# Performance work log

Measured on AMD Instinct MI355X. Metric: run time of the kernel, lower is better.

## Reference

```python
import jax, jax.numpy as jnp
import numpy as np

N_NODES = 50000


def gcn_layer(x, src, dst, ew, W, b, n_nodes):
    # PyG GCNConv: add self-loops (weight 1), symmetric deg^-1/2 normalization,
    # linear transform, scatter-add aggregation at destination, then bias.
    loop = jnp.arange(n_nodes, dtype=src.dtype)
    s = jnp.concatenate([src, loop])
    d = jnp.concatenate([dst, loop])
    w = jnp.concatenate([ew, jnp.ones((n_nodes,), dtype=ew.dtype)])
    deg = jax.ops.segment_sum(w, d, num_segments=n_nodes)  # [N]
    dinv = jnp.where(deg > 0, jax.lax.rsqrt(jnp.where(deg > 0, deg, 1.0)), 0.0)
    norm = dinv[s] * w * dinv[d]  # [E+N]
    h = x @ W  # [N, out]
    msg = h[s] * norm[:, None]  # gather + scale, [E+N, out]
    out = jax.ops.segment_sum(msg, d, num_segments=n_nodes)  # scatter-add
    return out + b


def setup_inputs() -> dict:
    key = jax.random.key(0)
    k1, k2, k3, k4, k5, k6, k7 = jax.random.split(key, 7)
    N, E, C_IN, C_OUT = N_NODES, 600000, 128, 128
    x = jax.random.normal(k1, (N, C_IN), dtype=jnp.float32)
    edge_index = jax.random.randint(k2, (2, E), 0, N, dtype=jnp.int64)
    edge_weight = jax.random.uniform(k3, (E,), dtype=jnp.float32)
    # Glorot-style init like PyG's Linear default
    s1 = 1.0 / np.sqrt(C_IN)
    s2 = 1.0 / np.sqrt(C_OUT)
    W1 = jax.random.uniform(k4, (C_IN, C_OUT), jnp.float32, -s1, s1)
    b1 = jnp.zeros((C_OUT,), dtype=jnp.float32)
    W2 = jax.random.uniform(k5, (C_OUT, C_OUT), jnp.float32, -s2, s2)
    b2 = jnp.zeros((C_OUT,), dtype=jnp.float32)
    return {"x": x, "edge_index": edge_index, "edge_weight": edge_weight,
            "W1": W1, "b1": b1, "W2": W2, "b2": b2}


def reference(x, edge_index, edge_weight, W1, b1, W2, b2):
    src, dst = edge_index[0], edge_index[1]
    h = jax.nn.relu(gcn_layer(x, src, dst, edge_weight, W1, b1, N_NODES))
    return jax.nn.relu(gcn_layer(h, src, dst, edge_weight, W2, b2, N_NODES))
```

## Files before the change

### kernel.cpp

```cpp
#include <hip/hip_runtime.h>
#include <math.h>

#define CH   128
#define CH4  32
#define TPB  256
#define SCANB 1024
#define WIMG 16384
#define NREP 8
#define FIXS 1048576.0f

typedef __attribute__((ext_vector_type(8))) short short8;
typedef __attribute__((ext_vector_type(4))) float floatx4;
typedef __attribute__((ext_vector_type(8))) float float8;
typedef unsigned long long u64;

static __device__ __forceinline__ unsigned short f2bf(float f) {
    unsigned u = __float_as_uint(f);
    return (unsigned short)((u + 0x7fffu + ((u >> 16) & 1u)) >> 16);
}
static __device__ __forceinline__ float bf2f(unsigned short s) {
    return __uint_as_float(((unsigned)s) << 16);
}
static __device__ __forceinline__ float8 bf8_to_f8(short8 u) {
    float8 f;
    #pragma unroll
    for (int i = 0; i < 8; ++i) f[i] = bf2f((unsigned short)u[i]);
    return f;
}
static __device__ __forceinline__ int xcc_id() {
    int x;
    asm volatile("s_getreg_b32 %0, hwreg(HW_REG_XCC_ID)" : "=s"(x));
    return x & (NREP - 1);
}

__global__ void k_prep(const float* __restrict__ W1, const float* __restrict__ W2,
                       short* __restrict__ Wsplit, float4* __restrict__ zbase,
                       int nzero4, int nbPrep) {
    int bx = blockIdx.x;
    if (bx >= nbPrep) {
        int i = (bx - nbPrep) * TPB + threadIdx.x;
        if (i < nzero4) zbase[i] = make_float4(0.f, 0.f, 0.f, 0.f);
        return;
    }
    int i = bx * TPB + threadIdx.x;
    if (i >= 2 * CH * CH) return;
    int layer = i >> 14;
    int idx   = i & 16383;
    int k = idx >> 7, c = idx & 127;
    float w = (layer ? W2 : W1)[k * CH + c];
    unsigned short hi = f2bf(w);
    unsigned short lo = f2bf(w - bf2f(hi));
    int colh = c >> 6, nn = c & 63;
    int kt = k >> 5, q = (k & 31) >> 3, j = k & 7;
    int ns = nn >> 4, ln = q * 16 + (nn & 15);
    size_t base = (size_t)(layer * 2 + colh) * WIMG;
    size_t off  = ((size_t)(kt * 4 + ns) * 64 + ln) * 8 + j;
    Wsplit[base + off]        = (short)hi;
    Wsplit[base + 8192 + off] = (short)lo;
}

static __device__ __forceinline__ void gemm_body_f32(
        const float* __restrict__ X, const short* __restrict__ Wfrag,
        unsigned short* __restrict__ H, int n, int tile, int colh, int tid) {
    __shared__ __align__(16) short sW[2][4][4][64][8];
    {
        const float4* gsrc = (const float4*)Wfrag;
        float4* ldst = (float4*)sW;
        #pragma unroll
        for (int i = 0; i < 8; ++i)
            ldst[i * TPB + tid] = gsrc[i * TPB + tid];
    }
    __syncthreads();

    const int lane = tid & 63;
    const int wv   = tid >> 6;
    const int q    = lane >> 4;
    const int m    = lane & 15;
    const int row0 = tile * 64 + wv * 16;
    if (row0 >= n) return;

    int rrow = row0 + m;
    if (rrow > n - 1) rrow = n - 1;

    const float4* xr = (const float4*)(X + (size_t)rrow * CH);
    float4 xa[4][2];
    #pragma unroll
    for (int kt = 0; kt < 4; ++kt) {
        xa[kt][0] = xr[kt * 8 + q * 2 + 0];
        xa[kt][1] = xr[kt * 8 + q * 2 + 1];
    }

    floatx4 acc[4];
    #pragma unroll
    for (int ns = 0; ns < 4; ++ns) acc[ns] = (floatx4){0.f, 0.f, 0.f, 0.f};

    #pragma unroll
    for (int kt = 0; kt < 4; ++kt) {
        float xf[8] = { xa[kt][0].x, xa[kt][0].y, xa[kt][0].z, xa[kt][0].w,
                        xa[kt][1].x, xa[kt][1].y, xa[kt][1].z, xa[kt][1].w };
        short8 ah, al;
        #pragma unroll
        for (int j = 0; j < 8; ++j) {
            float v = xf[j];
            unsigned short h = f2bf(v);
            ah[j] = (short)h;
            al[j] = (short)f2bf(v - bf2f(h));
        }
        #pragma unroll
        for (int ns = 0; ns < 4; ++ns) {
            short8 bh = *(const short8*)&sW[0][kt][ns][lane][0];
            short8 bl = *(const short8*)&sW[1][kt][ns][lane][0];
            acc[ns] = __builtin_amdgcn_mfma_f32_16x16x32_bf16(ah, bh, acc[ns], 0, 0, 0);
            acc[ns] = __builtin_amdgcn_mfma_f32_16x16x32_bf16(al, bh, acc[ns], 0, 0, 0);
            acc[ns] = __builtin_amdgcn_mfma_f32_16x16x32_bf16(ah, bl, acc[ns], 0, 0, 0);
        }
    }

    #pragma unroll
    for (int ns = 0; ns < 4; ++ns) {
        #pragma unroll
        for (int reg = 0; reg < 4; ++reg) {
            int r = row0 + q * 4 + reg;
            if (r < n)
                H[(size_t)r * CH + colh * 64 + ns * 16 + m] = f2bf(acc[ns][reg]);
        }
    }
}

__global__ __launch_bounds__(TPB, 4)
void k_gemm_rank(const float* __restrict__ X, const short* __restrict__ Wsplit,
                 unsigned short* __restrict__ H, int n,
                 const int* __restrict__ dst, const float* __restrict__ ew,
                 u64* __restrict__ counts_rep, int* __restrict__ rank,
                 int E, int nbE4, int Np) {
    int bx = blockIdx.x;
    if (bx < nbE4) {
        const int rep = xcc_id();
        int stride = nbE4 * TPB;
        int e = bx * TPB + threadIdx.x;
        #pragma unroll
        for (int it = 0; it < 4; ++it, e += stride) {
            if (e < E) {
                int d = dst[e];
                if ((unsigned)d < (unsigned)n) {
                    u64 pk = (1ull << 40) |
                             (u64)(unsigned)__float2uint_rn(ew[e] * FIXS);
                    u64 old = atomicAdd(&counts_rep[(size_t)rep * Np + d], pk);
                    rank[e] = (rep << 28) | (int)(old >> 40);
                }
            }
        }
    } else {
        bx -= nbE4;
        int colh = bx & 1;
        gemm_body_f32(X, Wsplit + (size_t)colh * WIMG, H, n, bx >> 1, colh,
                      threadIdx.x);
    }
}

__global__ __launch_bounds__(SCANB)
void k_scan1(const u64* __restrict__ counts_rep, int Np,
             int* __restrict__ counts_tot, int* __restrict__ repoff8,
             int* __restrict__ row_start, float* __restrict__ dinv,
             int* __restrict__ partials, int* __restrict__ pp_s,
             int* __restrict__ done, int nb, int n) {
    __shared__ int swt[SCANB / 64];
    __shared__ int slastS;
    const int tid  = threadIdx.x;
    const int lane = tid & 63;
    const int wid  = tid >> 6;
    const int gid  = blockIdx.x * SCANB + tid;

    int c[NREP];
    int v = 0;
    u64 wsum = 0;
    #pragma unroll
    for (int r = 0; r < NREP; ++r) {
        u64 pk = (gid < n) ? counts_rep[(size_t)r * Np + gid] : 0ull;
        c[r] = (int)(pk >> 40);
        wsum += pk & ((1ull << 40) - 1);
        v += c[r];
    }
    const int vp = (v + 7) & ~7;
    int inc = vp;
    #pragma unroll
    for (int off = 1; off < 64; off <<= 1) {
        int t = __shfl_up(inc, off, 64);
        if (lane >= off) inc += t;
    }
    if (lane == 63) swt[wid] = inc;
    __syncthreads();
    if (wid == 0) {
        int wv_ = (lane < SCANB / 64) ? swt[lane] : 0;
        int winc = wv_;
        #pragma unroll
        for (int off = 1; off < SCANB / 64; off <<= 1) {
            int t = __shfl_up(winc, off, 64);
            if (lane >= off) winc += t;
        }
        if (lane < SCANB / 64) swt[lane] = winc - wv_;
    }
    __syncthreads();
    const int myincl = inc + swt[wid];

    if (gid < n) {
        row_start[gid]  = myincl - vp;
        counts_tot[gid] = v;
        dinv[gid] = rsqrtf(1.0f + (float)wsum * (1.0f / FIXS));
        int pre = 0;
        int ro[NREP];
        #pragma unroll
        for (int r = 0; r < NREP; ++r) { ro[r] = pre; pre += c[r]; }
        ((int4*)repoff8)[gid * 2 + 0] = make_int4(ro[0], ro[1], ro[2], ro[3]);
        ((int4*)repoff8)[gid * 2 + 1] = make_int4(ro[4], ro[5], ro[6], ro[7]);
    }
    if (tid == SCANB - 1) {
        partials[blockIdx.x] = myincl;
        __threadfence();
        int old = atomicAdd(done, 1);
        slastS = (old == nb - 1);
    }
    __syncthreads();
    if (slastS && tid < 64) {
        int pv = (tid < nb) ? atomicAdd(&partials[tid], 0) : 0;
        int i2 = pv;
        #pragma unroll
        for (int off = 1; off < 64; off <<= 1) {
            int t = __shfl_up(i2, off, 64);
            if ((tid & 63) >= off) i2 += t;
        }
        if (tid < nb) pp_s[tid] = i2 - pv;
    }
}

__global__ void k_fill(const int* __restrict__ src, const int* __restrict__ dst,
                       const float* __restrict__ ew, const int* __restrict__ row_start,
                       const int* __restrict__ pp_s, const int* __restrict__ repoff8,
                       const int* __restrict__ rank, const float* __restrict__ dinv,
                       const int* __restrict__ counts_tot,
                       int2* __restrict__ edges, int E, int n, int nbE) {
    int bx = blockIdx.x;
    if (bx >= nbE) {
        int node = (bx - nbE) * TPB + threadIdx.x;
        if (node >= n) return;
        int v  = counts_tot[node];
        int vp = (v + 7) & ~7;
        if (v == vp) return;
        int base = row_start[node] + pp_s[node >> 10] + v;
        for (int k = 0; k < vp - v; ++k)
            edges[base + k] = make_int2(0, 0);
        return;
    }
    int e = bx * TPB + threadIdx.x;
    if (e >= E) return;
    int s = src[e], d = dst[e];
    if ((unsigned)s >= (unsigned)n || (unsigned)d >= (unsigned)n) return;
    int rr   = rank[e];
    int rep  = (rr >> 28) & (NREP - 1);
    int slot = rr & 0x0FFFFFFF;
    int base = row_start[d] + pp_s[d >> 10] + repoff8[d * NREP + rep];
    edges[base + slot] = make_int2(s, __float_as_int(ew[e] * dinv[s]));
}

static __device__ __forceinline__ float8 agg_node8(
        const short8* __restrict__ h8, const int2* __restrict__ edges,
        float di, const float8 b, int node, int tx,
        const int* __restrict__ row_start, const int* __restrict__ pp_s,
        const int* __restrict__ counts) {
    float8 hv = bf8_to_f8(h8[(size_t)node * 16 + tx]);
    float8 acc;
    #pragma unroll
    for (int i = 0; i < 8; ++i) acc[i] = 0.f;

    int j   = row_start[node] + pp_s[node >> 10];
    int end = j + ((counts[node] + 7) & ~7);

    for (; j < end; j += 8) {
        int2 e[8];
        #pragma unroll
        for (int i = 0; i < 8; ++i) e[i] = edges[j + i];
        short8 g[8];
        #pragma unroll
        for (int i = 0; i < 8; ++i) g[i] = h8[(size_t)e[i].x * 16 + tx];
        #pragma unroll
        for (int i = 0; i < 8; ++i) {
            float w = __int_as_float(e[i].y);
            float8 gf = bf8_to_f8(g[i]);
            #pragma unroll
            for (int c = 0; c < 8; ++c) acc[c] += gf[c] * w;
        }
    }

    float di2 = di * di;
    float8 o;
    #pragma unroll
    for (int c = 0; c < 8; ++c) o[c] = di2 * hv[c] + di * acc[c] + b[c];
    return o;
}

__global__ __launch_bounds__(TPB)
void k_agg_gemm(const unsigned short* __restrict__ h,
                const int* __restrict__ row_start, const int* __restrict__ pp_s,
                const int* __restrict__ counts, const int2* __restrict__ edges,
                const float* __restrict__ dinv, const float* __restrict__ bias,
                const short* __restrict__ W2img,
                unsigned short* __restrict__ h2, int n) {
    __shared__ __align__(16) short8 tile[16 * 17];
    const int tid = threadIdx.x;

    const int bnode0 = (int)blockIdx.x * 16;
    const int tx = tid & 15;
    const int tg = tid >> 4;
    const int node = bnode0 + tg;
    float8 b;
    #pragma unroll
    for (int c = 0; c < 8; ++c) b[c] = bias[tx * 8 + c];
    short8 u;
    if (node < n) {
        float8 o = agg_node8((const short8*)h, edges, dinv[node], b, node,
                             tx, row_start, pp_s, counts);
        #pragma unroll
        for (int c = 0; c < 8; ++c) u[c] = (short)f2bf(fmaxf(o[c], 0.f));
    } else {
        #pragma unroll
        for (int c = 0; c < 8; ++c) u[c] = 0;
    }
    tile[tg * 17 + tx] = u;
    __syncthreads();

    const int lane = tid & 63;
    const int wv   = tid >> 6;
    const int q    = lane >> 4;
    const int m    = lane & 15;
    const int ch   = wv & 1;
    const int ns0  = (wv >> 1) * 2;

    short8 a[4];
    #pragma unroll
    for (int kt = 0; kt < 4; ++kt)
        a[kt] = tile[m * 17 + kt * 4 + q];

    const short8* w2f = (const short8*)(W2img + (size_t)ch * WIMG);

    floatx4 acc[2];
    #pragma unroll
    for (int i = 0; i < 2; ++i) acc[i] = (floatx4){0.f, 0.f, 0.f, 0.f};

    #pragma unroll
    for (int kt = 0; kt < 4; ++kt) {
        #pragma unroll
        for (int i = 0; i < 2; ++i) {
            short8 bh = w2f[(kt * 4 + ns0 + i) * 64 + lane];
            acc[i] = __builtin_amdgcn_mfma_f32_16x16x32_bf16(a[kt], bh, acc[i],
                                                             0, 0, 0);
        }
    }

    #pragma unroll
    for (int i = 0; i < 2; ++i)
        #pragma unroll
        for (int reg = 0; reg < 4; ++reg) {
            int r = bnode0 + q * 4 + reg;
            if (r < n)
                h2[(size_t)r * CH + ch * 64 + (ns0 + i) * 16 + m] =
                    f2bf(acc[i][reg]);
        }
}

__global__ __launch_bounds__(TPB)
void k_aggregate2(const unsigned short* __restrict__ h,
                  const int* __restrict__ row_start, const int* __restrict__ pp_s,
                  const int* __restrict__ counts, const int2* __restrict__ edges,
                  const float* __restrict__ dinv, const float* __restrict__ bias,
                  float* __restrict__ out, int n) {
    int t = blockIdx.x * blockDim.x + threadIdx.x;
    int node = t >> 4;
    if (node >= n) return;
    int tx = t & 15;
    float8 b;
    #pragma unroll
    for (int c = 0; c < 8; ++c) b[c] = bias[tx * 8 + c];
    float8 o = agg_node8((const short8*)h, edges, dinv[node], b, node, tx,
                         row_start, pp_s, counts);
    float4 lo = make_float4(fmaxf(o[0], 0.f), fmaxf(o[1], 0.f),
                            fmaxf(o[2], 0.f), fmaxf(o[3], 0.f));
    float4 hi = make_float4(fmaxf(o[4], 0.f), fmaxf(o[5], 0.f),
                            fmaxf(o[6], 0.f), fmaxf(o[7], 0.f));
    ((float4*)out)[(size_t)node * CH4 + tx * 2 + 0] = lo;
    ((float4*)out)[(size_t)node * CH4 + tx * 2 + 1] = hi;
}

extern "C" void kernel_launch(void* const* d_in, const int* in_sizes, int n_in,
                              void* d_out, int out_size, void* d_ws, size_t ws_size,
                              hipStream_t stream) {
    const float* x  = (const float*)d_in[0];
    const int*   ei = (const int*)d_in[1];
    const float* ew = (const float*)d_in[2];
    const float* W1 = (const float*)d_in[3];
    const float* b1 = (const float*)d_in[4];
    const float* W2 = (const float*)d_in[5];
    const float* b2 = (const float*)d_in[6];
    float* out = (float*)d_out;

    const int N = in_sizes[0] / CH;
    const int E = in_sizes[2];
    const int* src = ei;
    const int* dst = ei + E;

    size_t Np   = ((size_t)N + 255) & ~(size_t)255;
    size_t Ep   = ((size_t)E + 63) & ~(size_t)63;
    size_t Epad = (size_t)E + 8 * Np;
    float* ws          = (float*)d_ws;
    float* dinv        = ws;
    unsigned short* h  = (unsigned short*)(dinv + Np);
    unsigned short* h2 = h + (size_t)N * CH;
    u64*   counts_rep  = (u64*)(h2 + (size_t)N * CH);
    int*   done        = (int*)(counts_rep + NREP * Np);
    int    nzero4      = (int)((2 * NREP * Np + 64) / 4);
    int*  counts_tot   = done + 64;
    int*  row_start    = counts_tot + Np;
    int*  repoff8      = row_start + Np;
    int*  rank         = repoff8 + NREP * Np;
    int*  partials     = rank + Ep;
    int*  pp_s         = partials + 64;
    int2* edges        = (int2*)(pp_s + 64);
    short* Wsplit      = (short*)(edges + Epad);

    const int nbE    = (E + TPB - 1) / TPB;
    const int nbN    = (N + TPB - 1) / TPB;
    const int nbE4   = (E + TPB * 4 - 1) / (TPB * 4);
    const int nbAgg  = (int)(((size_t)N * 16 + TPB - 1) / TPB);
    const int nbScan = (N + SCANB - 1) / SCANB;
    const int nbGemm = 2 * ((N + 63) / 64);
    const int nbAG   = (N + 15) / 16;
    const int nbPrep = (2 * CH * CH + TPB - 1) / TPB;
    const int nbZero = (nzero4 + TPB - 1) / TPB;

    k_prep     <<<nbPrep + nbZero, TPB, 0, stream>>>(W1, W2, Wsplit,
                                                     (float4*)counts_rep,
                                                     nzero4, nbPrep);

    k_gemm_rank<<<nbE4 + nbGemm, TPB, 0, stream>>>(x, Wsplit, h, N, dst, ew,
                                                   counts_rep, rank, E, nbE4,
                                                   (int)Np);
    k_scan1    <<<nbScan, SCANB, 0, stream>>>(counts_rep, (int)Np, counts_tot,
                                              repoff8, row_start, dinv,
                                              partials, pp_s, done, nbScan, N);
    k_fill     <<<nbE + nbN, TPB, 0, stream>>>(src, dst, ew, row_start, pp_s,
                                               repoff8, rank, dinv, counts_tot,
                                               edges, E, N, nbE);

    k_agg_gemm <<<nbAG, TPB, 0, stream>>>(h, row_start, pp_s, counts_tot,
                                          edges, dinv, b1,
                                          Wsplit + 2 * (size_t)WIMG, h2, N);
    k_aggregate2<<<nbAgg, TPB, 0, stream>>>(h2, row_start, pp_s, counts_tot,
                                            edges, dinv, b2, out, N);
}
```

Measured before the change: 200.4 us.

## Bin nodes by padded degree and process aggregation in degree-sorted order

During the scan, each node is placed into one of four bins by its padded in-degree using an atomic counter, building a permutation array. Both aggregation kernels map their linear index through this permutation, so nodes with similar degree share a wavefront and a block, which is meant to reduce lane divergence and load imbalance in the gather loops. In exchange it adds atomics in the scan, an extra indirection per node, and scattered output writes, and it loses node locality in h2/out stores.

```diff
diff --git a/kernel.cpp b/kernel.cpp
--- a/kernel.cpp
+++ b/kernel.cpp
@@ -31,6 +31,18 @@
     int x;
     asm volatile("s_getreg_b32 %0, hwreg(HW_REG_XCC_ID)" : "=s"(x));
     return x & (NREP - 1);
+}
+static __device__ __forceinline__ int map_node(
+        int fi, int n, const int* __restrict__ bincnt,
+        const int* __restrict__ perm, int Np) {
+    int c0 = bincnt[0], c1 = bincnt[1], c2 = bincnt[2];
+    int bin, local;
+    if (fi < c0)                { bin = 0; local = fi; }
+    else if (fi < c0 + c1)      { bin = 1; local = fi - c0; }
+    else if (fi < c0 + c1 + c2) { bin = 2; local = fi - c0 - c1; }
+    else                        { bin = 3; local = fi - c0 - c1 - c2; }
+    int node = perm[(size_t)bin * Np + local];
+    return ((unsigned)node < (unsigned)n) ? node : 0;
 }
 
 __global__ void k_prep(const float* __restrict__ W1, const float* __restrict__ W2,
@@ -163,7 +175,8 @@
              int* __restrict__ counts_tot, int* __restrict__ repoff8,
              int* __restrict__ row_start, float* __restrict__ dinv,
              int* __restrict__ partials, int* __restrict__ pp_s,
-             int* __restrict__ done, int nb, int n) {
+             int* __restrict__ done, int* __restrict__ bincnt,
+             int* __restrict__ perm, int nb, int n) {
     __shared__ int swt[SCANB / 64];
     __shared__ int slastS;
     const int tid  = threadIdx.x;
@@ -213,6 +226,9 @@
         for (int r = 0; r < NREP; ++r) { ro[r] = pre; pre += c[r]; }
         ((int4*)repoff8)[gid * 2 + 0] = make_int4(ro[0], ro[1], ro[2], ro[3]);
         ((int4*)repoff8)[gid * 2 + 1] = make_int4(ro[4], ro[5], ro[6], ro[7]);
+        int bin = vp >> 3; if (bin > 3) bin = 3;
+        int slot = atomicAdd(&bincnt[bin], 1);
+        if (slot < Np) perm[(size_t)bin * Np + slot] = gid;
     }
     if (tid == SCANB - 1) {
         partials[blockIdx.x] = myincl;
@@ -304,19 +320,22 @@
                 const int* __restrict__ counts, const int2* __restrict__ edges,
                 const float* __restrict__ dinv, const float* __restrict__ bias,
                 const short* __restrict__ W2img,
-                unsigned short* __restrict__ h2, int n) {
+                const int* __restrict__ bincnt, const int* __restrict__ perm,
+                int Np, unsigned short* __restrict__ h2, int n) {
     __shared__ __align__(16) short8 tile[16 * 17];
+    __shared__ int smap[16];
     const int tid = threadIdx.x;
 
-    const int bnode0 = (int)blockIdx.x * 16;
     const int tx = tid & 15;
     const int tg = tid >> 4;
-    const int node = bnode0 + tg;
+    const int fi = (int)blockIdx.x * 16 + tg;
+    int node = (fi < n) ? map_node(fi, n, bincnt, perm, Np) : -1;
+    if (tx == 0) smap[tg] = node;
     float8 b;
     #pragma unroll
     for (int c = 0; c < 8; ++c) b[c] = bias[tx * 8 + c];
     short8 u;
-    if (node < n) {
+    if (node >= 0) {
         float8 o = agg_node8((const short8*)h, edges, dinv[node], b, node,
                              tx, row_start, pp_s, counts);
         #pragma unroll
@@ -360,9 +379,9 @@
     for (int i = 0; i < 2; ++i)
         #pragma unroll
         for (int reg = 0; reg < 4; ++reg) {
-            int r = bnode0 + q * 4 + reg;
-            if (r < n)
-                h2[(size_t)r * CH + ch * 64 + (ns0 + i) * 16 + m] =
+            int rnode = smap[q * 4 + reg];
+            if (rnode >= 0)
+                h2[(size_t)rnode * CH + ch * 64 + (ns0 + i) * 16 + m] =
                     f2bf(acc[i][reg]);
         }
 }
@@ -372,11 +391,13 @@
                   const int* __restrict__ row_start, const int* __restrict__ pp_s,
                   const int* __restrict__ counts, const int2* __restrict__ edges,
                   const float* __restrict__ dinv, const float* __restrict__ bias,
-                  float* __restrict__ out, int n) {
+                  const int* __restrict__ bincnt, const int* __restrict__ perm,
+                  int Np, float* __restrict__ out, int n) {
     int t = blockIdx.x * blockDim.x + threadIdx.x;
-    int node = t >> 4;
-    if (node >= n) return;
+    int fi = t >> 4;
+    if (fi >= n) return;
     int tx = t & 15;
+    int node = map_node(fi, n, bincnt, perm, Np);
     float8 b;
     #pragma unroll
     for (int c = 0; c < 8; ++c) b[c] = bias[tx * 8 + c];
@@ -416,12 +437,14 @@
     unsigned short* h2 = h + (size_t)N * CH;
     u64*   counts_rep  = (u64*)(h2 + (size_t)N * CH);
     int*   done        = (int*)(counts_rep + NREP * Np);
-    int    nzero4      = (int)((2 * NREP * Np + 64) / 4);
-    int*  counts_tot   = done + 64;
+    int*   bincnt      = done + 64;
+    int    nzero4      = (int)((2 * NREP * Np + 128) / 4);
+    int*  counts_tot   = bincnt + 64;
     int*  row_start    = counts_tot + Np;
     int*  repoff8      = row_start + Np;
     int*  rank         = repoff8 + NREP * Np;
-    int*  partials     = rank + Ep;
+    int*  perm         = rank + Ep;
+    int*  partials     = perm + 4 * Np;
     int*  pp_s         = partials + 64;
     int2* edges        = (int2*)(pp_s + 64);
     short* Wsplit      = (short*)(edges + Epad);
@@ -445,14 +468,17 @@
                                                    (int)Np);
     k_scan1    <<<nbScan, SCANB, 0, stream>>>(counts_rep, (int)Np, counts_tot,
                                               repoff8, row_start, dinv,
-                                              partials, pp_s, done, nbScan, N);
+                                              partials, pp_s, done, bincnt,
+                                              perm, nbScan, N);
     k_fill     <<<nbE + nbN, TPB, 0, stream>>>(src, dst, ew, row_start, pp_s,
                                                repoff8, rank, dinv, counts_tot,
                                                edges, E, N, nbE);
 
     k_agg_gemm <<<nbAG, TPB, 0, stream>>>(h, row_start, pp_s, counts_tot,
                                           edges, dinv, b1,
-                                          Wsplit + 2 * (size_t)WIMG, h2, N);
+                                          Wsplit + 2 * (size_t)WIMG,
+                                          bincnt, perm, (int)Np, h2, N);
     k_aggregate2<<<nbAgg, TPB, 0, stream>>>(h2, row_start, pp_s, counts_tot,
-                                            edges, dinv, b2, out, N);
-}
+                                            edges, dinv, b2, bincnt, perm,
+                                            (int)Np, out, N);
+}
```

New measurement: 629.3 us. +214.0%, slower.
